# Optimization experiments

Hardware: AMD Instinct MI355X
Metric: run time of the kernel (lower is better)

## Reference

```python
import jax, jax.numpy as jnp
import numpy as np

B, T, E = 128, 8, 52
S, R, L = 2048, 512, 4
VOCAB = 512


def setup_inputs() -> dict:
    key = jax.random.key(0)
    ks = jax.random.split(key, 16)
    enc_len = jax.random.randint(ks[5], (B,), 0, S, dtype=jnp.int32)
    enc_len = jnp.maximum(enc_len, 1)  # ragged lengths >= 1
    return {
        "featEmbed": jax.random.normal(ks[0], (B, T, E), jnp.float32),
        "labelsEmbed": jax.random.normal(ks[1], (B, T, E), jnp.float32),
        "encoder_outputs": jax.random.normal(ks[2], (B, S, R), jnp.float32),
        "h_n": jax.random.normal(ks[3], (B, R), jnp.float32),
        "mask": jax.random.randint(ks[4], (B, T), 0, 2, dtype=jnp.int32),
        "enc_len": enc_len,
        "emb_feat_table": jax.random.normal(ks[6], (VOCAB, E), jnp.float32) * 0.1,
        "W_fc_pool": jax.random.normal(ks[7], (L, R), jnp.float32) * (1.0 / np.sqrt(R)),
        "W_reg": jax.random.normal(ks[8], (L, R), jnp.float32) * (1.0 / np.sqrt(R)),
        "b_reg": jax.random.normal(ks[9], (L,), jnp.float32) * 0.01,
        "W_ih": jax.random.normal(ks[10], (3 * R, 2 * E), jnp.float32) * (1.0 / np.sqrt(2 * E)),
        "W_hh": jax.random.normal(ks[11], (3 * R, R), jnp.float32) * (1.0 / np.sqrt(R)),
        "b_ih": jax.random.normal(ks[12], (3 * R,), jnp.float32) * 0.01,
        "b_hh": jax.random.normal(ks[13], (3 * R,), jnp.float32) * 0.01,
    }


# label -> feature-vocab remap (dict d in original forward)
REMAP = jnp.array([175, 176, 44, 173], dtype=jnp.int32)


def _gru_cell(x, h, W_ih, W_hh, b_ih, b_hh):
    # PyTorch nn.GRUCell semantics
    gi = x @ W_ih.T + b_ih  # [B, 3R]
    gh = h @ W_hh.T + b_hh
    i_r, i_z, i_n = jnp.split(gi, 3, axis=1)
    h_r, h_z, h_nn = jnp.split(gh, 3, axis=1)
    r = jax.nn.sigmoid(i_r + h_r)
    z = jax.nn.sigmoid(i_z + h_z)
    n = jnp.tanh(i_n + r * h_nn)
    return (1.0 - z) * n + z * h


def reference(featEmbed, labelsEmbed, encoder_outputs, h_n, mask, enc_len,
              emb_feat_table, W_fc_pool, W_reg, b_reg, W_ih, W_hh, b_ih, b_hh):
    S_ = encoder_outputs.shape[1]
    # Ragged max-pool over valid encoder positions (replaces per-sample AdaptiveMaxPool1d loop)
    valid = jnp.arange(S_)[None, :] < enc_len[:, None]          # [B, S]
    neg = jnp.finfo(encoder_outputs.dtype).min
    code_pool = jnp.max(jnp.where(valid[:, :, None], encoder_outputs, neg), axis=1)  # [B, R]
    a = code_pool @ W_fc_pool.T                                  # [B, L]; constant over t

    def step(h, inp):
        x, bmi_t, m = inp                                        # [B,E], [B,E], [B]
        bmi_h = h @ W_reg.T + b_reg + a                          # [B, L]
        bmi_prob = jax.nn.sigmoid(bmi_h)
        bmi_label = jnp.argmax(bmi_prob, axis=1)                 # [B]
        label_dict = REMAP[bmi_label]                            # host-dict remap, vectorized
        bmi_label_enc = emb_feat_table[label_dict]               # [B, E]
        mf = m.astype(x.dtype)[:, None]
        bmi = bmi_t * mf + (1.0 - mf) * bmi_label_enc
        h_new = _gru_cell(jnp.concatenate([x, bmi], axis=1), h, W_ih, W_hh, b_ih, b_hh)
        return h_new, (bmi_label, bmi_prob, bmi_h, label_dict)

    xs = (jnp.swapaxes(featEmbed, 0, 1),    # [T,B,E]
          jnp.swapaxes(labelsEmbed, 0, 1),  # [T,B,E]
          mask.T)                            # [T,B]
    _, (dec_output, dec_prob, disc_input, kl_input) = jax.lax.scan(step, h_n, xs)
    L_ = dec_prob.shape[-1]
    # dec_output: [T,B] labels; dec_prob: [T,B,L]; disc_input: [T*B,L]; kl_input: [T*B]
    return dec_output, dec_prob, disc_input.reshape(-1, L_), kl_input.reshape(-1)
```

## Files before the change

kernel.cpp:

```cpp
#include <hip/hip_runtime.h>
#include <hip/hip_bf16.h>
#include <float.h>
#include <math.h>


#define B_ 128
#define T_ 8
#define E_ 52
#define S_ 2048
#define R_ 512
#define L_ 4
#define GR_ 1536
#define KX_ 104
#define NCHUNK 16
#define SCHUNK (S_ / NCHUNK)
#define KQ_ 154

__device__ __constant__ int c_remap[4] = {175, 176, 44, 173};

__device__ __forceinline__ float sigmoidf(float x) { return 1.0f / (1.0f + expf(-x)); }

__global__ void k_maxpool(const float* __restrict__ enc, const int* __restrict__ enc_len,
                          float4* __restrict__ partial) {
    int c = blockIdx.x;
    int b = blockIdx.y;
    int t = threadIdx.x;
    int len = enc_len[b];
    int s0 = c * SCHUNK;
    int s1 = min(s0 + SCHUNK, len);
    float4 m = make_float4(-FLT_MAX, -FLT_MAX, -FLT_MAX, -FLT_MAX);
    const float4* base = (const float4*)(enc + (size_t)b * S_ * R_);
    for (int s = s0; s < s1; ++s) {
        float4 v = base[(size_t)s * (R_ / 4) + t];
        m.x = fmaxf(m.x, v.x);
        m.y = fmaxf(m.y, v.y);
        m.z = fmaxf(m.z, v.z);
        m.w = fmaxf(m.w, v.w);
    }
    partial[((size_t)b * NCHUNK + c) * (R_ / 4) + t] = m;
}

__global__ void k_pool_a(const float* __restrict__ partial, const float* __restrict__ W_fc,
                         float* __restrict__ a_out) {
    int b = blockIdx.x;
    int tid = threadIdx.x;
    __shared__ float cp[R_];
    for (int r = tid; r < R_; r += 256) {
        float m = -FLT_MAX;
        const float* p = partial + (size_t)b * NCHUNK * R_ + r;
        #pragma unroll
        for (int c = 0; c < NCHUNK; ++c) m = fmaxf(m, p[c * R_]);
        cp[r] = m;
    }
    __syncthreads();
    float p0 = 0.f, p1 = 0.f, p2 = 0.f, p3 = 0.f;
    for (int r = tid; r < R_; r += 256) {
        float v = cp[r];
        p0 = fmaf(v, W_fc[0 * R_ + r], p0);
        p1 = fmaf(v, W_fc[1 * R_ + r], p1);
        p2 = fmaf(v, W_fc[2 * R_ + r], p2);
        p3 = fmaf(v, W_fc[3 * R_ + r], p3);
    }
    #pragma unroll
    for (int off = 32; off > 0; off >>= 1) {
        p0 += __shfl_down(p0, off);
        p1 += __shfl_down(p1, off);
        p2 += __shfl_down(p2, off);
        p3 += __shfl_down(p3, off);
    }
    __shared__ float red[4][4];
    int wv = tid >> 6, lane = tid & 63;
    if (lane == 0) { red[wv][0] = p0; red[wv][1] = p1; red[wv][2] = p2; red[wv][3] = p3; }
    __syncthreads();
    if (tid < 4) {
        a_out[b * L_ + tid] = red[0][tid] + red[1][tid] + red[2][tid] + red[3][tid];
    }
}

__global__ void k_transpose2(const float* __restrict__ Wih, const float* __restrict__ Whh,
                             float* __restrict__ WihT, float* __restrict__ WhhT) {
    const float* in = blockIdx.z ? Whh : Wih;
    float* outp = blockIdx.z ? WhhT : WihT;
    int kdim = blockIdx.z ? R_ : KX_;
    if (blockIdx.x * 32 >= kdim) return;
    __shared__ float tile[32][33];
    int j0 = blockIdx.x * 32;
    int i0 = blockIdx.y * 32;
    int tx = threadIdx.x, ty = threadIdx.y;
    #pragma unroll
    for (int dy = 0; dy < 32; dy += 8) {
        int i = i0 + ty + dy, j = j0 + tx;
        if (j < kdim) tile[ty + dy][tx] = in[(size_t)i * kdim + j];
    }
    __syncthreads();
    #pragma unroll
    for (int dy = 0; dy < 32; dy += 8) {
        int j = j0 + ty + dy, i = i0 + tx;
        if (j < kdim) outp[(size_t)j * GR_ + i] = tile[tx][ty + dy];
    }
}

__global__ void __launch_bounds__(1024, 1) k_step(
        const float* __restrict__ h, const float* __restrict__ W_reg,
        const float* __restrict__ b_reg, const float* __restrict__ a_vec,
        const float* __restrict__ featEmbed, const float* __restrict__ labelsEmbed,
        const int* __restrict__ mask, const float* __restrict__ emb_table,
        const float* __restrict__ WihT, const float* __restrict__ WhhT,
        const float* __restrict__ b_ih, const float* __restrict__ b_hh,
        int t, float* __restrict__ h_out, float* __restrict__ out) {
    int tid = threadIdx.x;
    int lane = tid & 63;
    int w = tid >> 6;
    int bb = w >> 2;
    int q = w & 3;
    int b = blockIdx.y * 4 + bb;
    int rr = blockIdx.x * 64 + lane;

    __shared__ float xs[4][KX_];
    __shared__ float red[4][3][64][4];

    if (w < 4) {
        int bp = blockIdx.y * 4 + w;
        const float* hb = h + bp * R_;
        float p0 = 0.f, p1 = 0.f, p2 = 0.f, p3 = 0.f;
        #pragma unroll
        for (int r = lane; r < R_; r += 64) {
            float v = hb[r];
            p0 = fmaf(v, W_reg[r], p0);
            p1 = fmaf(v, W_reg[512 + r], p1);
            p2 = fmaf(v, W_reg[1024 + r], p2);
            p3 = fmaf(v, W_reg[1536 + r], p3);
        }
        #pragma unroll
        for (int off = 32; off > 0; off >>= 1) {
            p0 += __shfl_down(p0, off);
            p1 += __shfl_down(p1, off);
            p2 += __shfl_down(p2, off);
            p3 += __shfl_down(p3, off);
        }
        p0 = __shfl(p0, 0); p1 = __shfl(p1, 0); p2 = __shfl(p2, 0); p3 = __shfl(p3, 0);
        float bh[4];
        bh[0] = p0 + b_reg[0] + a_vec[bp * 4 + 0];
        bh[1] = p1 + b_reg[1] + a_vec[bp * 4 + 1];
        bh[2] = p2 + b_reg[2] + a_vec[bp * 4 + 2];
        bh[3] = p3 + b_reg[3] + a_vec[bp * 4 + 3];
        float pr[4];
        #pragma unroll
        for (int l = 0; l < 4; ++l) pr[l] = sigmoidf(bh[l]);
        int best = 0;
        float bv = pr[0];
        #pragma unroll
        for (int l = 1; l < 4; ++l) {
            if (pr[l] > bv) { bv = pr[l]; best = l; }
        }
        int ld = c_remap[best];
        if (blockIdx.x == 0 && lane == 0) {
            out[t * B_ + bp] = (float)best;
            #pragma unroll
            for (int l = 0; l < 4; ++l) {
                out[1024 + (t * B_ + bp) * 4 + l] = pr[l];
                out[5120 + (t * B_ + bp) * 4 + l] = bh[l];
            }
            out[9216 + t * B_ + bp] = (float)ld;
        }
        if (lane < E_) {
            xs[w][lane] = featEmbed[bp * (T_ * E_) + t * E_ + lane];
            int m = mask[bp * T_ + t];
            xs[w][E_ + lane] = m ? labelsEmbed[bp * (T_ * E_) + t * E_ + lane]
                                 : emb_table[ld * E_ + lane];
        }
    }
    __syncthreads();

    float ar = 0.f, az = 0.f, ain = 0.f, ahn = 0.f;
    int k0 = q * KQ_, k1 = k0 + KQ_;
    int xe = min(k1, KX_);
    #pragma unroll 4
    for (int k = k0; k < xe; ++k) {
        float x = xs[bb][k];
        const float* wp = WihT + (size_t)k * GR_ + rr;
        ar = fmaf(x, wp[0], ar);
        az = fmaf(x, wp[512], az);
        ain = fmaf(x, wp[1024], ain);
    }
    const float* hrow = h + b * R_;
    int hs = max(k0, KX_) - KX_;
    int he = k1 - KX_;
    #pragma unroll 4
    for (int k = hs; k < he; ++k) {
        float hv = hrow[k];
        const float* wp = WhhT + (size_t)k * GR_ + rr;
        ar = fmaf(hv, wp[0], ar);
        az = fmaf(hv, wp[512], az);
        ahn = fmaf(hv, wp[1024], ahn);
    }
    if (q != 0) {
        red[bb][q - 1][lane][0] = ar;
        red[bb][q - 1][lane][1] = az;
        red[bb][q - 1][lane][2] = ain;
        red[bb][q - 1][lane][3] = ahn;
    }
    __syncthreads();
    if (q == 0) {
        #pragma unroll
        for (int j = 0; j < 3; ++j) {
            ar += red[bb][j][lane][0];
            az += red[bb][j][lane][1];
            ain += red[bb][j][lane][2];
            ahn += red[bb][j][lane][3];
        }
        float r = sigmoidf(ar + b_ih[rr] + b_hh[rr]);
        float z = sigmoidf(az + b_ih[rr + 512] + b_hh[rr + 512]);
        float n = tanhf(ain + b_ih[rr + 1024] + r * (ahn + b_hh[rr + 1024]));
        h_out[b * R_ + rr] = (1.0f - z) * n + z * hrow[rr];
    }
}

extern "C" void kernel_launch(void* const* d_in, const int* in_sizes, int n_in,
                              void* d_out, int out_size, void* d_ws, size_t ws_size,
                              hipStream_t stream) {
    const float* featEmbed   = (const float*)d_in[0];
    const float* labelsEmbed = (const float*)d_in[1];
    const float* enc         = (const float*)d_in[2];
    const float* h_n         = (const float*)d_in[3];
    const int*   mask        = (const int*)d_in[4];
    const int*   enc_len     = (const int*)d_in[5];
    const float* emb_table   = (const float*)d_in[6];
    const float* W_fc        = (const float*)d_in[7];
    const float* W_reg       = (const float*)d_in[8];
    const float* b_reg       = (const float*)d_in[9];
    const float* W_ih        = (const float*)d_in[10];
    const float* W_hh        = (const float*)d_in[11];
    const float* b_ih        = (const float*)d_in[12];
    const float* b_hh        = (const float*)d_in[13];
    float* out = (float*)d_out;

    float* ws      = (float*)d_ws;
    float* partial = ws;
    float* WihT    = partial + B_ * NCHUNK * R_;
    float* WhhT    = WihT + KX_ * GR_;
    float* h0      = WhhT + R_ * GR_;
    float* h1      = h0 + B_ * R_;
    float* a_vec   = h1 + B_ * R_;

    k_transpose2<<<dim3(16, GR_ / 32, 2), dim3(32, 8), 0, stream>>>(W_ih, W_hh, WihT, WhhT);
    k_maxpool<<<dim3(NCHUNK, B_), 128, 0, stream>>>(enc, enc_len, (float4*)partial);
    k_pool_a<<<B_, 256, 0, stream>>>(partial, W_fc, a_vec);

    const float* hcur = h_n;
    for (int t = 0; t < T_; ++t) {
        float* hnext = (t & 1) ? h1 : h0;
        k_step<<<dim3(R_ / 64, B_ / 4), 1024, 0, stream>>>(
            hcur, W_reg, b_reg, a_vec, featEmbed, labelsEmbed, mask, emb_table,
            WihT, WhhT, b_ih, b_hh, t, hnext, out);
        hcur = hnext;
    }
}
```

Measured before the change: 877.5 us.

## Reuse packed float4 GRU weights across four batch rows per wave

Repacks W_ih and W_hh into a K-quad interleaved float4 layout. Each wave in the step kernel now computes all four batch rows of the block over a 1/16 slice of K, so every weight load is reused four times. Hidden states are staged in shared memory, and a multi-stage shared-memory tree reduction merges the 16 partial accumulators. This cuts repeated weight traffic from cache, at the cost of more registers per thread and several extra barriers.

```diff
diff --git a/kernel.cpp b/kernel.cpp
--- a/kernel.cpp
+++ b/kernel.cpp
@@ -1,5 +1,4 @@
 #include <hip/hip_runtime.h>
-#include <hip/hip_bf16.h>
 #include <float.h>
 #include <math.h>
 
@@ -14,11 +13,19 @@
 #define KX_ 104
 #define NCHUNK 16
 #define SCHUNK (S_ / NCHUNK)
-#define KQ_ 154
+#define NQ_ 154
+#define XQ_ 26
 
 __device__ __constant__ int c_remap[4] = {175, 176, 44, 173};
 
 __device__ __forceinline__ float sigmoidf(float x) { return 1.0f / (1.0f + expf(-x)); }
+__device__ __forceinline__ float dot4(float4 w, float4 x, float a) {
+    a = fmaf(w.x, x.x, a);
+    a = fmaf(w.y, x.y, a);
+    a = fmaf(w.z, x.z, a);
+    a = fmaf(w.w, x.w, a);
+    return a;
+}
 
 __global__ void k_maxpool(const float* __restrict__ enc, const int* __restrict__ enc_len,
                           float4* __restrict__ partial) {
@@ -77,26 +84,17 @@
     }
 }
 
-__global__ void k_transpose2(const float* __restrict__ Wih, const float* __restrict__ Whh,
-                             float* __restrict__ WihT, float* __restrict__ WhhT) {
-    const float* in = blockIdx.z ? Whh : Wih;
-    float* outp = blockIdx.z ? WhhT : WihT;
-    int kdim = blockIdx.z ? R_ : KX_;
-    if (blockIdx.x * 32 >= kdim) return;
-    __shared__ float tile[32][33];
-    int j0 = blockIdx.x * 32;
-    int i0 = blockIdx.y * 32;
-    int tx = threadIdx.x, ty = threadIdx.y;
+__global__ void k_pack(const float* __restrict__ Wih, const float* __restrict__ Whh,
+                       float4* __restrict__ Wp) {
+    int qd = blockIdx.x;
+    int rr = threadIdx.x;
     #pragma unroll
-    for (int dy = 0; dy < 32; dy += 8) {
-        int i = i0 + ty + dy, j = j0 + tx;
-        if (j < kdim) tile[ty + dy][tx] = in[(size_t)i * kdim + j];
-    }
-    __syncthreads();
-    #pragma unroll
-    for (int dy = 0; dy < 32; dy += 8) {
-        int j = j0 + ty + dy, i = i0 + tx;
-        if (j < kdim) outp[(size_t)j * GR_ + i] = tile[tx][ty + dy];
+    for (int g = 0; g < 3; ++g) {
+        int row = g * 512 + rr;
+        float4 v;
+        if (qd < XQ_) v = *(const float4*)(Wih + (size_t)row * KX_ + 4 * qd);
+        else          v = *(const float4*)(Whh + (size_t)row * R_  + 4 * (qd - XQ_));
+        Wp[((size_t)qd * 3 + g) * 512 + rr] = v;
     }
 }
 
@@ -105,23 +103,30 @@
         const float* __restrict__ b_reg, const float* __restrict__ a_vec,
         const float* __restrict__ featEmbed, const float* __restrict__ labelsEmbed,
         const int* __restrict__ mask, const float* __restrict__ emb_table,
-        const float* __restrict__ WihT, const float* __restrict__ WhhT,
-        const float* __restrict__ b_ih, const float* __restrict__ b_hh,
+        const float4* __restrict__ Wp, const float* __restrict__ b_ih,
+        const float* __restrict__ b_hh,
         int t, float* __restrict__ h_out, float* __restrict__ out) {
     int tid = threadIdx.x;
     int lane = tid & 63;
     int w = tid >> 6;
-    int bb = w >> 2;
-    int q = w & 3;
-    int b = blockIdx.y * 4 + bb;
+    int b0 = blockIdx.y * 4;
     int rr = blockIdx.x * 64 + lane;
 
-    __shared__ float xs[4][KX_];
-    __shared__ float red[4][3][64][4];
+    __shared__ __align__(16) float xs[4][KX_];
+    __shared__ __align__(16) float hs[4][R_];
+    __shared__ float red[8][64][17];
+
+    if (w >= 4 && w < 8) {
+        int bi = w - 4;
+        const float4* src = (const float4*)(h + (size_t)(b0 + bi) * R_);
+        float4* dst = (float4*)hs[bi];
+        dst[lane] = src[lane];
+        dst[lane + 64] = src[lane + 64];
+    }
 
     if (w < 4) {
-        int bp = blockIdx.y * 4 + w;
-        const float* hb = h + bp * R_;
+        int bp = b0 + w;
+        const float* hb = h + (size_t)bp * R_;
         float p0 = 0.f, p1 = 0.f, p2 = 0.f, p3 = 0.f;
         #pragma unroll
         for (int r = lane; r < R_; r += 64) {
@@ -172,47 +177,99 @@
     }
     __syncthreads();
 
-    float ar = 0.f, az = 0.f, ain = 0.f, ahn = 0.f;
-    int k0 = q * KQ_, k1 = k0 + KQ_;
-    int xe = min(k1, KX_);
-    #pragma unroll 4
-    for (int k = k0; k < xe; ++k) {
-        float x = xs[bb][k];
-        const float* wp = WihT + (size_t)k * GR_ + rr;
-        ar = fmaf(x, wp[0], ar);
-        az = fmaf(x, wp[512], az);
-        ain = fmaf(x, wp[1024], ain);
-    }
-    const float* hrow = h + b * R_;
-    int hs = max(k0, KX_) - KX_;
-    int he = k1 - KX_;
-    #pragma unroll 4
-    for (int k = hs; k < he; ++k) {
-        float hv = hrow[k];
-        const float* wp = WhhT + (size_t)k * GR_ + rr;
-        ar = fmaf(hv, wp[0], ar);
-        az = fmaf(hv, wp[512], az);
-        ahn = fmaf(hv, wp[1024], ahn);
-    }
-    if (q != 0) {
-        red[bb][q - 1][lane][0] = ar;
-        red[bb][q - 1][lane][1] = az;
-        red[bb][q - 1][lane][2] = ain;
-        red[bb][q - 1][lane][3] = ahn;
-    }
-    __syncthreads();
-    if (q == 0) {
-        #pragma unroll
-        for (int j = 0; j < 3; ++j) {
-            ar += red[bb][j][lane][0];
-            az += red[bb][j][lane][1];
-            ain += red[bb][j][lane][2];
-            ahn += red[bb][j][lane][3];
-        }
-        float r = sigmoidf(ar + b_ih[rr] + b_hh[rr]);
-        float z = sigmoidf(az + b_ih[rr + 512] + b_hh[rr + 512]);
-        float n = tanhf(ain + b_ih[rr + 1024] + r * (ahn + b_hh[rr + 1024]));
-        h_out[b * R_ + rr] = (1.0f - z) * n + z * hrow[rr];
+    float acc[16];
+    #pragma unroll
+    for (int j = 0; j < 16; ++j) acc[j] = 0.f;
+
+    int q0 = (NQ_ * w) >> 4;
+    int q1 = (NQ_ * (w + 1)) >> 4;
+    const float4* wp0 = Wp + (size_t)q0 * 1536 + rr;
+
+    int xe = min(q1, XQ_);
+    #pragma unroll 2
+    for (int qd = q0; qd < xe; ++qd) {
+        float4 wr = wp0[0];
+        float4 wz = wp0[512];
+        float4 wn = wp0[1024];
+        wp0 += 1536;
+        #pragma unroll
+        for (int bi = 0; bi < 4; ++bi) {
+            float4 xv = *(const float4*)&xs[bi][4 * qd];
+            acc[0 + bi]  = dot4(wr, xv, acc[0 + bi]);
+            acc[4 + bi]  = dot4(wz, xv, acc[4 + bi]);
+            acc[8 + bi]  = dot4(wn, xv, acc[8 + bi]);
+        }
+    }
+    int hq0 = max(q0, XQ_);
+    #pragma unroll 2
+    for (int qd = hq0; qd < q1; ++qd) {
+        float4 wr = wp0[0];
+        float4 wz = wp0[512];
+        float4 wn = wp0[1024];
+        wp0 += 1536;
+        int hq = 4 * (qd - XQ_);
+        #pragma unroll
+        for (int bi = 0; bi < 4; ++bi) {
+            float4 xv = *(const float4*)&hs[bi][hq];
+            acc[0 + bi]  = dot4(wr, xv, acc[0 + bi]);
+            acc[4 + bi]  = dot4(wz, xv, acc[4 + bi]);
+            acc[12 + bi] = dot4(wn, xv, acc[12 + bi]);
+        }
+    }
+
+    if (w >= 8) {
+        float* d = red[w - 8][lane];
+        #pragma unroll
+        for (int j = 0; j < 16; ++j) d[j] = acc[j];
+    }
+    __syncthreads();
+    if (w < 8) {
+        const float* s = red[w][lane];
+        #pragma unroll
+        for (int j = 0; j < 16; ++j) acc[j] += s[j];
+    }
+    if (w >= 4 && w < 8) {
+        float* d = red[w][lane];
+        #pragma unroll
+        for (int j = 0; j < 16; ++j) d[j] = acc[j];
+    }
+    __syncthreads();
+    if (w < 4) {
+        const float* s = red[w + 4][lane];
+        #pragma unroll
+        for (int j = 0; j < 16; ++j) acc[j] += s[j];
+    }
+    if (w >= 2 && w < 4) {
+        float* d = red[w][lane];
+        #pragma unroll
+        for (int j = 0; j < 16; ++j) d[j] = acc[j];
+    }
+    __syncthreads();
+    if (w < 2) {
+        const float* s = red[w + 2][lane];
+        #pragma unroll
+        for (int j = 0; j < 16; ++j) acc[j] += s[j];
+    }
+    if (w == 1) {
+        float* d = red[1][lane];
+        #pragma unroll
+        for (int j = 0; j < 16; ++j) d[j] = acc[j];
+    }
+    __syncthreads();
+    if (w == 0) {
+        const float* s = red[1][lane];
+        #pragma unroll
+        for (int j = 0; j < 16; ++j) acc[j] += s[j];
+        float bir = b_ih[rr],        bhr = b_hh[rr];
+        float biz = b_ih[512 + rr],  bhz = b_hh[512 + rr];
+        float bin = b_ih[1024 + rr], bhn = b_hh[1024 + rr];
+        #pragma unroll
+        for (int bi = 0; bi < 4; ++bi) {
+            float r = sigmoidf(acc[0 + bi] + bir + bhr);
+            float z = sigmoidf(acc[4 + bi] + biz + bhz);
+            float n = tanhf(acc[8 + bi] + bin + r * (acc[12 + bi] + bhn));
+            h_out[(size_t)(b0 + bi) * R_ + rr] = (1.0f - z) * n + z * hs[bi][rr];
+        }
     }
 }
 
@@ -237,13 +294,12 @@
 
     float* ws      = (float*)d_ws;
     float* partial = ws;
-    float* WihT    = partial + B_ * NCHUNK * R_;
-    float* WhhT    = WihT + KX_ * GR_;
-    float* h0      = WhhT + R_ * GR_;
+    float* Wp      = partial + B_ * NCHUNK * R_;
+    float* h0      = Wp + NQ_ * 3 * R_ * 4;
     float* h1      = h0 + B_ * R_;
     float* a_vec   = h1 + B_ * R_;
 
-    k_transpose2<<<dim3(16, GR_ / 32, 2), dim3(32, 8), 0, stream>>>(W_ih, W_hh, WihT, WhhT);
+    k_pack<<<dim3(NQ_), 512, 0, stream>>>(W_ih, W_hh, (float4*)Wp);
     k_maxpool<<<dim3(NCHUNK, B_), 128, 0, stream>>>(enc, enc_len, (float4*)partial);
     k_pool_a<<<B_, 256, 0, stream>>>(partial, W_fc, a_vec);
 
@@ -252,7 +308,7 @@
         float* hnext = (t & 1) ? h1 : h0;
         k_step<<<dim3(R_ / 64, B_ / 4), 1024, 0, stream>>>(
             hcur, W_reg, b_reg, a_vec, featEmbed, labelsEmbed, mask, emb_table,
-            WihT, WhhT, b_ih, b_hh, t, hnext, out);
+            (const float4*)Wp, b_ih, b_hh, t, hnext, out);
         hcur = hnext;
     }
 }
```

After: 773.9 us. -11.8%, faster.
